# Kernel tuning notes

Measured on AMD Instinct MI355X. Metric: run time of the kernel, lower is better.

Reference implementation:

```python
import jax, jax.numpy as jnp
import numpy as np

N_WIRES = 8
DIM = 2 ** N_WIRES  # 256
NUM_HEADS = 4

def _cnot_ring_perm():
    # Compose CNOT(w, w+1) for w=0..6 then CNOT(7, 0) into one basis permutation.
    # Wire 0 is the most-significant bit of the basis index.
    perm = np.arange(DIM)
    pairs = [(w, w + 1) for w in range(N_WIRES - 1)] + [(N_WIRES - 1, 0)]
    j = np.arange(DIM)
    for c, t in pairs:
        ctrl = (j >> (N_WIRES - 1 - c)) & 1
        M = j ^ (ctrl << (N_WIRES - 1 - t))  # flip target bit where control=1 (involution)
        perm = perm[M]
    return perm

PERM = _cnot_ring_perm()
# SIGNS[i, w] = <i|Z_w|i> = 1 - 2*bit_w(i)
SIGNS = np.array([[1.0 - 2.0 * ((i >> (N_WIRES - 1 - w)) & 1) for w in range(N_WIRES)]
                  for i in range(DIM)], dtype=np.float32)

def setup_inputs() -> dict:
    key = jax.random.key(0)
    k1, k2, k3 = jax.random.split(key, 3)
    x = jax.random.normal(k1, (16, 4096, N_WIRES), jnp.float32)  # rotation angles per token
    theta = jax.random.normal(k2, (N_WIRES,), jnp.float32)       # trainable RX params
    w_combine = jax.random.normal(k3, (N_WIRES, N_WIRES), jnp.float32) / np.float32(np.sqrt(N_WIRES))
    b_combine = jnp.zeros((N_WIRES,), jnp.float32)
    return {"x": x, "theta": theta, "w_combine": w_combine, "b_combine": b_combine}

def _quantum_features(x, theta):
    # RX(x_i) then RX(theta_i) on wire i compose to RX(x_i + theta_i) acting on |0>.
    B, S, E = x.shape
    N = B * S
    phi = (x + theta).reshape(N, E)
    c = jnp.cos(0.5 * phi).astype(jnp.complex64)
    s = (-1j) * jnp.sin(0.5 * phi)          # RX|0> = cos(phi/2)|0> - i sin(phi/2)|1>
    wv = jnp.stack([c, s.astype(jnp.complex64)], axis=-1)  # (N, 8, 2)
    # Build product state via successive Kronecker products (wire 0 = MSB).
    state = jnp.ones((N, 1), jnp.complex64)
    for w in range(E):
        state = (state[:, :, None] * wv[:, w, None, :]).reshape(N, -1)  # (N, 2^(w+1))
    state = state[:, jnp.asarray(PERM)]      # apply the CNOT ring as one permutation
    probs = state.real ** 2 + state.imag ** 2  # (N, 256)
    return (probs @ jnp.asarray(SIGNS)).reshape(B, S, E)  # <Z_w> per token

def reference(x, theta, w_combine, b_combine):
    B, S, E = x.shape
    d_k = E // NUM_HEADS
    q = _quantum_features(x, theta)           # (B, S, 8); k = v = q in the source
    scores = jnp.einsum('bse,bte->bst', q, q) / np.float32(np.sqrt(d_k))
    attn = jax.nn.softmax(scores, axis=-1)    # dropout is identity in eval mode
    out = jnp.einsum('bst,bte->bse', attn, q)
    # Faithful to source: transpose(1,2).contiguous().view(B, S, E)
    out = jnp.swapaxes(out, 1, 2).reshape(B, S, E)
    return out @ w_combine.T + b_combine
```

## Files before the change

kernel.cpp:

```cpp
#include <hip/hip_runtime.h>
#include <math.h>


#define SEQ   4096
#define NB    16
#define SROWS 128
#define TPB   1024
#define NTG   4
#define TC    1024
#define NCH   (SEQ / TC)
#define TILES_PER_TG 8
#define KSTR  12
#define VSTR  1028

typedef _Float16 f16x4  __attribute__((ext_vector_type(4)));
typedef _Float16 f16x8  __attribute__((ext_vector_type(8)));
typedef float    f32x16 __attribute__((ext_vector_type(16)));
typedef __fp16   hf2    __attribute__((ext_vector_type(2)));

#if __has_builtin(__builtin_amdgcn_exp2f)
#define EXP2F(x) __builtin_amdgcn_exp2f(x)
#else
#define EXP2F(x) exp2f(x)
#endif

__global__ __launch_bounds__(TPB, 8)
void qattn_kernel(const float* __restrict__ x, const float* __restrict__ theta,
                  const float* __restrict__ wc, const float* __restrict__ bc,
                  float* __restrict__ out)
{
    __shared__ __align__(16) _Float16 kf[TC * KSTR];
    __shared__ __align__(16) _Float16 vt[9 * VSTR];
    float* part = (float*)kf;
    float* attn = (float*)vt;

    const int tid  = threadIdx.x;
    const int lane = tid & 63;
    const int wv   = tid >> 6;
    const int sub  = wv & 3;
    const int tg   = wv >> 2;
    const int l31  = lane & 31;
    const int hp   = lane >> 5;

    const int b  = blockIdx.x >> 5;
    const int S0 = (blockIdx.x & 31) * SROWS;
    const float* xb = x + (size_t)b * SEQ * 8;

    float th[8];
#pragma unroll
    for (int w = 0; w < 8; ++w) th[w] = theta[w];

    vt[8 * VSTR + tid] = (_Float16)1.0f;

    f16x8 qfrag = {(_Float16)0.f, (_Float16)0.f, (_Float16)0.f, (_Float16)0.f,
                   (_Float16)0.f, (_Float16)0.f, (_Float16)0.f, (_Float16)0.f};
    {
        const int s = S0 + sub * 32 + l31;
        const float4 xa  = *(const float4*)(xb + s * 8);
        const float4 xb4 = *(const float4*)(xb + s * 8 + 4);
        float c0 = __cosf(xa.x  + th[0]);
        float c1 = __cosf(xa.y  + th[1]);
        float c2 = __cosf(xa.z  + th[2]);
        float c3 = __cosf(xa.w  + th[3]);
        float c4 = __cosf(xb4.x + th[4]);
        float c5 = __cosf(xb4.y + th[5]);
        float c6 = __cosf(xb4.z + th[6]);
        float c7 = __cosf(xb4.w + th[7]);
        float p1 = c0 * c1, p2 = p1 * c2, p3 = p2 * c3, p4 = p3 * c4;
        float p5 = p4 * c5, p6 = p5 * c6, p7 = p6 * c7;
        float p0 = c1 * c2 * c3 * c4 * c5 * c6 * c7;
        const float sc = 0.70710678118654752f * 1.44269504088896341f;
        if (hp == 0)
            qfrag = (f16x8){(_Float16)(p0*sc), (_Float16)(p1*sc),
                            (_Float16)(p2*sc), (_Float16)(p3*sc),
                            (_Float16)(p4*sc), (_Float16)(p5*sc),
                            (_Float16)(p6*sc), (_Float16)(p7*sc)};
    }

    const f32x16 Z = {0.f,0.f,0.f,0.f,0.f,0.f,0.f,0.f,
                      0.f,0.f,0.f,0.f,0.f,0.f,0.f,0.f};
    f32x16 o = Z;

    const int wr = (l31 < 8) ? l31 : 8;
    const _Float16* kfb = kf + l31 * KSTR + (tg * TILES_PER_TG) * 32 * KSTR;
    const _Float16* vbb = vt + wr * VSTR + 4 * hp + tg * (TILES_PER_TG * 32);

    for (int ch = 0; ch < NCH; ++ch) {
        __syncthreads();
        {
            const int t = ch * TC + tid;
            const float4 xa  = *(const float4*)(xb + t * 8);
            const float4 xb4 = *(const float4*)(xb + t * 8 + 4);
            float c0 = __cosf(xa.x  + th[0]);
            float c1 = __cosf(xa.y  + th[1]);
            float c2 = __cosf(xa.z  + th[2]);
            float c3 = __cosf(xa.w  + th[3]);
            float c4 = __cosf(xb4.x + th[4]);
            float c5 = __cosf(xb4.y + th[5]);
            float c6 = __cosf(xb4.z + th[6]);
            float c7 = __cosf(xb4.w + th[7]);
            float p1 = c0 * c1, p2 = p1 * c2, p3 = p2 * c3, p4 = p3 * c4;
            float p5 = p4 * c5, p6 = p5 * c6, p7 = p6 * c7;
            float p0 = c1 * c2 * c3 * c4 * c5 * c6 * c7;
            _Float16 h0 = (_Float16)p0, h1 = (_Float16)p1, h2 = (_Float16)p2,
                     h3 = (_Float16)p3, h4 = (_Float16)p4, h5 = (_Float16)p5,
                     h6 = (_Float16)p6, h7 = (_Float16)p7;
            _Float16* krow = kf + tid * KSTR;
            *(f16x4*)(krow)     = (f16x4){h0, h1, h2, h3};
            *(f16x4*)(krow + 4) = (f16x4){h4, h5, h6, h7};
            vt[0 * VSTR + tid] = h0;
            vt[1 * VSTR + tid] = h1;
            vt[2 * VSTR + tid] = h2;
            vt[3 * VSTR + tid] = h3;
            vt[4 * VSTR + tid] = h4;
            vt[5 * VSTR + tid] = h5;
            vt[6 * VSTR + tid] = h6;
            vt[7 * VSTR + tid] = h7;
        }
        __syncthreads();
#pragma unroll 2
        for (int i = 0; i < TILES_PER_TG; ++i) {
            const _Float16* kp = kfb + i * 32 * KSTR;
            union { f16x4 h[2]; f16x8 v; } kfr;
            kfr.h[0] = *(const f16x4*)(kp);
            kfr.h[1] = *(const f16x4*)(kp + 4);
            f32x16 cc = __builtin_amdgcn_mfma_f32_32x32x16_f16(kfr.v, qfrag, Z, 0, 0, 0);
            union { int i_[4]; f16x8 v; } A0, A1;
#pragma unroll
            for (int j = 0; j < 4; ++j) {
                union { hf2 h; int i_; } t2;
                t2.h = __builtin_amdgcn_cvt_pkrtz(EXP2F(cc[2*j]), EXP2F(cc[2*j+1]));
                A0.i_[j] = t2.i_;
                t2.h = __builtin_amdgcn_cvt_pkrtz(EXP2F(cc[8+2*j]), EXP2F(cc[8+2*j+1]));
                A1.i_[j] = t2.i_;
            }
            const _Float16* vp = vbb + i * 32;
            union { f16x4 h[2]; f16x8 v; } vf0, vf1;
            vf0.h[0] = *(const f16x4*)(vp);
            vf0.h[1] = *(const f16x4*)(vp + 8);
            vf1.h[0] = *(const f16x4*)(vp + 16);
            vf1.h[1] = *(const f16x4*)(vp + 24);
            o = __builtin_amdgcn_mfma_f32_32x32x16_f16(A0.v, vf0.v, o, 0, 0, 0);
            o = __builtin_amdgcn_mfma_f32_32x32x16_f16(A1.v, vf1.v, o, 0, 0, 0);
        }
    }

    __syncthreads();
    if (l31 < 9) {
#pragma unroll
        for (int r = 0; r < 16; ++r) {
            const int sloc = sub * 32 + (r & 3) + 8 * (r >> 2) + 4 * hp;
            part[((tg * SROWS) + sloc) * 9 + l31] = o[r];
        }
    }
    __syncthreads();
    for (int idx = tid; idx < SROWS * 9; idx += TPB) {
        const int rr = idx / 9;
        const int w  = idx - rr * 9;
        float sm = 0.f;
#pragma unroll
        for (int g = 0; g < NTG; ++g) sm += part[((g * SROWS) + rr) * 9 + w];
        attn[rr * 9 + w] = sm;
    }
    __syncthreads();
    if (tid < SROWS * 8) {
        const int rr = tid >> 3;
        const int w  = tid & 7;
        attn[rr * 9 + w] = attn[rr * 9 + w] / attn[rr * 9 + 8];
    }
    __syncthreads();

    if (tid < SROWS) {
        const int e    = tid >> 4;
        const int nloc = tid & 15;
        const int r    = e * 512 + (S0 >> 3) + nloc;
        float y[8];
#pragma unroll
        for (int c = 0; c < 8; ++c) y[c] = attn[(nloc * 8 + c) * 9 + e];
        float oo[8];
#pragma unroll
        for (int k = 0; k < 8; ++k) {
            float a = bc[k];
#pragma unroll
            for (int c = 0; c < 8; ++c) a += y[c] * wc[k * 8 + c];
            oo[k] = a;
        }
        float4* op = (float4*)(out + ((size_t)b * SEQ + r) * 8);
        op[0] = make_float4(oo[0], oo[1], oo[2], oo[3]);
        op[1] = make_float4(oo[4], oo[5], oo[6], oo[7]);
    }
}

extern "C" void kernel_launch(void* const* d_in, const int* in_sizes, int n_in,
                              void* d_out, int out_size, void* d_ws, size_t ws_size,
                              hipStream_t stream)
{
    const float* x  = (const float*)d_in[0];
    const float* th = (const float*)d_in[1];
    const float* wc = (const float*)d_in[2];
    const float* bc = (const float*)d_in[3];
    float* out = (float*)d_out;

    qattn_kernel<<<dim3(NB * (SEQ / SROWS)), dim3(TPB), 0, stream>>>(x, th, wc, bc, out);
}
```

Measured before the change: 91.94 us.

## Switch attention MFMAs to 16x16x32 tiles and halve rows per block

Replaces the 32x32x16 MFMA score and PV tiles with 16x16x32 MFMAs and halves the query rows per block from 128 to 64, doubling the grid. Each block still recomputes all key/value features for the whole sequence, so the feature-generation work per query row doubles. The aim is smaller MFMA tiles that waste less of the K=8 feature dimension and more blocks to spread across CUs. The risk is the duplicated cosine/LDS staging work per block.

New measurement: 97.38 us. +5.9%, slower.

```diff
diff --git a/kernel.cpp b/kernel.cpp
--- a/kernel.cpp
+++ b/kernel.cpp
@@ -4,19 +4,19 @@
 
 #define SEQ   4096
 #define NB    16
-#define SROWS 128
+#define SROWS 64
 #define TPB   1024
 #define NTG   4
 #define TC    1024
 #define NCH   (SEQ / TC)
-#define TILES_PER_TG 8
+#define PVG   8
 #define KSTR  12
 #define VSTR  1028
 
-typedef _Float16 f16x4  __attribute__((ext_vector_type(4)));
-typedef _Float16 f16x8  __attribute__((ext_vector_type(8)));
-typedef float    f32x16 __attribute__((ext_vector_type(16)));
-typedef __fp16   hf2    __attribute__((ext_vector_type(2)));
+typedef _Float16 f16x4 __attribute__((ext_vector_type(4)));
+typedef _Float16 f16x8 __attribute__((ext_vector_type(8)));
+typedef float    f32x4 __attribute__((ext_vector_type(4)));
+typedef __fp16   hf2   __attribute__((ext_vector_type(2)));
 
 #if __has_builtin(__builtin_amdgcn_exp2f)
 #define EXP2F(x) __builtin_amdgcn_exp2f(x)
@@ -39,11 +39,11 @@
     const int wv   = tid >> 6;
     const int sub  = wv & 3;
     const int tg   = wv >> 2;
-    const int l31  = lane & 31;
-    const int hp   = lane >> 5;
-
-    const int b  = blockIdx.x >> 5;
-    const int S0 = (blockIdx.x & 31) * SROWS;
+    const int l15  = lane & 15;
+    const int q    = lane >> 4;
+
+    const int b  = blockIdx.x >> 6;
+    const int S0 = (blockIdx.x & 63) * SROWS;
     const float* xb = x + (size_t)b * SEQ * 8;
 
     float th[8];
@@ -55,7 +55,7 @@
     f16x8 qfrag = {(_Float16)0.f, (_Float16)0.f, (_Float16)0.f, (_Float16)0.f,
                    (_Float16)0.f, (_Float16)0.f, (_Float16)0.f, (_Float16)0.f};
     {
-        const int s = S0 + sub * 32 + l31;
+        const int s = S0 + sub * 16 + l15;
         const float4 xa  = *(const float4*)(xb + s * 8);
         const float4 xb4 = *(const float4*)(xb + s * 8 + 4);
         float c0 = __cosf(xa.x  + th[0]);
@@ -70,20 +70,19 @@
         float p5 = p4 * c5, p6 = p5 * c6, p7 = p6 * c7;
         float p0 = c1 * c2 * c3 * c4 * c5 * c6 * c7;
         const float sc = 0.70710678118654752f * 1.44269504088896341f;
-        if (hp == 0)
+        if (q == 0)
             qfrag = (f16x8){(_Float16)(p0*sc), (_Float16)(p1*sc),
                             (_Float16)(p2*sc), (_Float16)(p3*sc),
                             (_Float16)(p4*sc), (_Float16)(p5*sc),
                             (_Float16)(p6*sc), (_Float16)(p7*sc)};
     }
 
-    const f32x16 Z = {0.f,0.f,0.f,0.f,0.f,0.f,0.f,0.f,
-                      0.f,0.f,0.f,0.f,0.f,0.f,0.f,0.f};
-    f32x16 o = Z;
-
-    const int wr = (l31 < 8) ? l31 : 8;
-    const _Float16* kfb = kf + l31 * KSTR + (tg * TILES_PER_TG) * 32 * KSTR;
-    const _Float16* vbb = vt + wr * VSTR + 4 * hp + tg * (TILES_PER_TG * 32);
+    const f32x4 Z = {0.f, 0.f, 0.f, 0.f};
+    f32x4 o = Z;
+
+    const int wr = (l15 < 8) ? l15 : 8;
+    const _Float16* kfb = kf + (tg * 256 + l15) * KSTR;
+    const _Float16* vbb = vt + wr * VSTR + tg * 256 + 4 * q;
 
     for (int ch = 0; ch < NCH; ++ch) {
         __syncthreads();
@@ -118,45 +117,43 @@
             vt[7 * VSTR + tid] = h7;
         }
         __syncthreads();
-#pragma unroll 2
-        for (int i = 0; i < TILES_PER_TG; ++i) {
-            const _Float16* kp = kfb + i * 32 * KSTR;
-            union { f16x4 h[2]; f16x8 v; } kfr;
-            kfr.h[0] = *(const f16x4*)(kp);
-            kfr.h[1] = *(const f16x4*)(kp + 4);
-            f32x16 cc = __builtin_amdgcn_mfma_f32_32x32x16_f16(kfr.v, qfrag, Z, 0, 0, 0);
-            union { int i_[4]; f16x8 v; } A0, A1;
-#pragma unroll
-            for (int j = 0; j < 4; ++j) {
+#pragma unroll
+        for (int pg = 0; pg < PVG; ++pg) {
+            const _Float16* kp = kfb + pg * 32 * KSTR;
+            union { f16x4 h[2]; f16x8 v; } k0, k1;
+            k0.h[0] = *(const f16x4*)(kp);
+            k0.h[1] = *(const f16x4*)(kp + 4);
+            k1.h[0] = *(const f16x4*)(kp + 16 * KSTR);
+            k1.h[1] = *(const f16x4*)(kp + 16 * KSTR + 4);
+            f32x4 cc0 = __builtin_amdgcn_mfma_f32_16x16x32_f16(k0.v, qfrag, Z, 0, 0, 0);
+            f32x4 cc1 = __builtin_amdgcn_mfma_f32_16x16x32_f16(k1.v, qfrag, Z, 0, 0, 0);
+            union { int i_[4]; f16x8 v; } A;
+            {
                 union { hf2 h; int i_; } t2;
-                t2.h = __builtin_amdgcn_cvt_pkrtz(EXP2F(cc[2*j]), EXP2F(cc[2*j+1]));
-                A0.i_[j] = t2.i_;
-                t2.h = __builtin_amdgcn_cvt_pkrtz(EXP2F(cc[8+2*j]), EXP2F(cc[8+2*j+1]));
-                A1.i_[j] = t2.i_;
+                t2.h = __builtin_amdgcn_cvt_pkrtz(EXP2F(cc0.x), EXP2F(cc0.y)); A.i_[0] = t2.i_;
+                t2.h = __builtin_amdgcn_cvt_pkrtz(EXP2F(cc0.z), EXP2F(cc0.w)); A.i_[1] = t2.i_;
+                t2.h = __builtin_amdgcn_cvt_pkrtz(EXP2F(cc1.x), EXP2F(cc1.y)); A.i_[2] = t2.i_;
+                t2.h = __builtin_amdgcn_cvt_pkrtz(EXP2F(cc1.z), EXP2F(cc1.w)); A.i_[3] = t2.i_;
             }
-            const _Float16* vp = vbb + i * 32;
-            union { f16x4 h[2]; f16x8 v; } vf0, vf1;
-            vf0.h[0] = *(const f16x4*)(vp);
-            vf0.h[1] = *(const f16x4*)(vp + 8);
-            vf1.h[0] = *(const f16x4*)(vp + 16);
-            vf1.h[1] = *(const f16x4*)(vp + 24);
-            o = __builtin_amdgcn_mfma_f32_32x32x16_f16(A0.v, vf0.v, o, 0, 0, 0);
-            o = __builtin_amdgcn_mfma_f32_32x32x16_f16(A1.v, vf1.v, o, 0, 0, 0);
-        }
-    }
-
-    __syncthreads();
-    if (l31 < 9) {
-#pragma unroll
-        for (int r = 0; r < 16; ++r) {
-            const int sloc = sub * 32 + (r & 3) + 8 * (r >> 2) + 4 * hp;
-            part[((tg * SROWS) + sloc) * 9 + l31] = o[r];
-        }
-    }
-    __syncthreads();
-    for (int idx = tid; idx < SROWS * 9; idx += TPB) {
-        const int rr = idx / 9;
-        const int w  = idx - rr * 9;
+            union { f16x4 h[2]; f16x8 v; } Bv;
+            Bv.h[0] = *(const f16x4*)(vbb + pg * 32);
+            Bv.h[1] = *(const f16x4*)(vbb + pg * 32 + 16);
+            o = __builtin_amdgcn_mfma_f32_16x16x32_f16(A.v, Bv.v, o, 0, 0, 0);
+        }
+    }
+
+    __syncthreads();
+    if (l15 < 9) {
+#pragma unroll
+        for (int r = 0; r < 4; ++r) {
+            const int sloc = sub * 16 + 4 * q + r;
+            part[((tg * SROWS) + sloc) * 9 + l15] = o[r];
+        }
+    }
+    __syncthreads();
+    if (tid < SROWS * 9) {
+        const int rr = tid / 9;
+        const int w  = tid - rr * 9;
         float sm = 0.f;
 #pragma unroll
         for (int g = 0; g < NTG; ++g) sm += part[((g * SROWS) + rr) * 9 + w];
@@ -171,8 +168,8 @@
     __syncthreads();
 
     if (tid < SROWS) {
-        const int e    = tid >> 4;
-        const int nloc = tid & 15;
+        const int e    = tid >> 3;
+        const int nloc = tid & 7;
         const int r    = e * 512 + (S0 >> 3) + nloc;
         float y[8];
 #pragma unroll
```
